# Kernel tuning notes

Hardware: AMD Instinct MI355X
Metric: run time of the kernel (lower is better)

Reference implementation:

```python
import jax, jax.numpy as jnp
import numpy as np

H = 16       # num_heads
DH = 64      # dim_head
SCALE = DH ** -0.5


def setup_inputs() -> dict:
    key = jax.random.key(0)
    k1, k2 = jax.random.split(key)
    ZT = jax.random.normal(k1, (2, 2048, 1024), dtype=jnp.float32)
    # Linear weight, shape (H*dh, dim); scaled like a typical init for stability
    W = jax.random.normal(k2, (1024, 1024), dtype=jnp.float32) * 0.02
    return {"ZT": ZT, "W": W}


def reference(ZT, W):
    b, n, dim = ZT.shape
    # UT(ZT): ZT @ W^T -> (b, n, H*dh), reshape to (b, h, n, dh)
    ZTU = jnp.einsum('bnd,ed->bne', ZT, W).reshape(b, n, H, DH).transpose(0, 2, 1, 3)
    # scores = ZTU @ ZTU^T * scale  (b, h, n, n)
    scores = jnp.einsum('bhnd,bhmd->bhnm', ZTU, ZTU) * SCALE
    attn = jax.nn.softmax(scores, axis=-1)  # dropout p=0 -> identity
    # attn @ ZTU -> (b, h, n, dh) -> (b, n, H*dh)
    ssa = jnp.einsum('bhnm,bhmd->bhnd', attn, ZTU)
    ssa = ssa.transpose(0, 2, 1, 3).reshape(b, n, H * DH)
    # UT(I).T == W (shape (H*dh, dim)); final projection back to dim
    mssa = jnp.einsum('bne,ed->bnd', ssa, W)
    # return_proj=False path: module returns (MSSA_out, MSSA_out)
    return (mssa, mssa)
```

## Files before the change

kernel.cpp:

```cpp
#include <hip/hip_runtime.h>
#include <hip/hip_bf16.h>
#include <stdint.h>

typedef __attribute__((ext_vector_type(8))) short bf16x8;
typedef __attribute__((ext_vector_type(4))) float f32x4;

#define MFMA16(a, b, c) __builtin_amdgcn_mfma_f32_16x16x32_bf16(a, b, c, 0, 0, 0)

typedef const __attribute__((address_space(1))) unsigned int* as1_u32p;
typedef __attribute__((address_space(3))) unsigned int* as3_u32p;
__device__ __forceinline__ void gl_lds16(const void* g, void* l) {
    __builtin_amdgcn_global_load_lds((as1_u32p)g, (as3_u32p)l, 16, 0, 0);
}

__device__ __forceinline__ unsigned short f2bs(float f) {
    __hip_bfloat16 h = __float2bfloat16(f);
    unsigned short s;
    __builtin_memcpy(&s, &h, 2);
    return s;
}

__device__ __forceinline__ unsigned int pk_bf16(float a, float b) {
    float2 f; f.x = a; f.y = b;
    __hip_bfloat162 h = __float22bfloat162_rn(f);
    unsigned int u;
    __builtin_memcpy(&u, &h, 4);
    return u;
}

__device__ __forceinline__ float exp2_raw(float x) {
    float r;
    asm("v_exp_f32 %0, %1" : "=v"(r) : "v"(x));
    return r;
}

#define QSCALE 0.18033688f

__global__ __launch_bounds__(256) void cvt_k(const float* __restrict__ w,
                                             const float* __restrict__ zt,
                                             unsigned short* __restrict__ wbf,
                                             unsigned short* __restrict__ wtbf,
                                             unsigned short* __restrict__ ztbf) {
    __shared__ __attribute__((aligned(16))) unsigned short T[64 * 72];
    const int tid = threadIdx.x;
    if (blockIdx.x >= 256) {
        const int i = ((int)blockIdx.x - 256) * 2048 + tid * 8;
        const float4 v0 = *(const float4*)(zt + i);
        const float4 v1 = *(const float4*)(zt + i + 4);
        uint4 wv;
        wv.x = pk_bf16(v0.x, v0.y);
        wv.y = pk_bf16(v0.z, v0.w);
        wv.z = pk_bf16(v1.x, v1.y);
        wv.w = pk_bf16(v1.z, v1.w);
        *(uint4*)(ztbf + i) = wv;
        return;
    }
    const int b2 = blockIdx.x;
    const int e0 = (b2 >> 4) * 64, d0 = (b2 & 15) * 64;
    const int el = tid >> 2;
    const int dl = (tid & 3) * 16;
    const float* src = w + (size_t)(e0 + el) * 1024 + d0 + dl;
    unsigned short myv[16];
#pragma unroll
    for (int q = 0; q < 4; ++q) {
        const float4 v = *(const float4*)(src + q * 4);
        myv[q * 4 + 0] = f2bs(v.x);
        myv[q * 4 + 1] = f2bs(v.y);
        myv[q * 4 + 2] = f2bs(v.z);
        myv[q * 4 + 3] = f2bs(v.w);
    }
    *(bf16x8*)(wbf + (size_t)(e0 + el) * 1024 + d0 + dl) = *(const bf16x8*)&myv[0];
    *(bf16x8*)(wbf + (size_t)(e0 + el) * 1024 + d0 + dl + 8) = *(const bf16x8*)&myv[8];
#pragma unroll
    for (int q = 0; q < 16; ++q) T[(dl + q) * 72 + el] = myv[q];
    __syncthreads();
#pragma unroll
    for (int p = 0; p < 2; ++p) {
        const int idx = p * 256 + tid;
        const int dd = idx >> 3, c = (idx & 7) * 8;
        const bf16x8 v = *(const bf16x8*)&T[dd * 72 + c];
        *(bf16x8*)(wtbf + (size_t)(d0 + dd) * 1024 + e0 + c) = v;
    }
}

template <int EPI>
__global__ __launch_bounds__(256, 2) void gemm_bt_k(
    const __hip_bfloat16* __restrict__ Abf, const __hip_bfloat16* __restrict__ B,
    unsigned short* __restrict__ ztu, unsigned short* __restrict__ ztut,
    float* __restrict__ out0, float* __restrict__ out1) {
    __shared__ __attribute__((aligned(16))) unsigned short smem[24576];
    unsigned short* Tb = smem;

    const int p = blockIdx.x;
    const int bm = (p & 7) * 8 + ((p >> 3) & 7);
    const int bn = p >> 6;
    const int tid = threadIdx.x;
    const int wave = tid >> 6, lane = tid & 63;
    const int wm = wave >> 1, wn = wave & 1;
    const int quad = lane >> 4, l16 = lane & 15;

    f32x4 acc[2][4] = {};

    const int lrow = lane >> 3;
    const int sw = (lane & 7) ^ lrow;
    const __hip_bfloat16* Ag0 = Abf + (size_t)(bm * 64 + (2 * wave) * 8 + lrow) * 1024 + sw * 8;
    const __hip_bfloat16* Ag1 = Ag0 + 8 * 1024;
    const __hip_bfloat16* Bg0 = B + (size_t)(bn * 128 + (4 * wave) * 8 + lrow) * 1024 + sw * 8;
    const __hip_bfloat16* Bg1 = Bg0 + 8 * 1024;
    const __hip_bfloat16* Bg2 = Bg0 + 16 * 1024;
    const __hip_bfloat16* Bg3 = Bg0 + 24 * 1024;

    auto stage = [&](int ko, unsigned short* sb) {
        gl_lds16(Ag0 + ko, sb + (2 * wave) * 512);
        gl_lds16(Ag1 + ko, sb + (2 * wave + 1) * 512);
        gl_lds16(Bg0 + ko, sb + 4096 + (4 * wave) * 512);
        gl_lds16(Bg1 + ko, sb + 4096 + (4 * wave + 1) * 512);
        gl_lds16(Bg2 + ko, sb + 4096 + (4 * wave + 2) * 512);
        gl_lds16(Bg3 + ko, sb + 4096 + (4 * wave + 3) * 512);
    };

    const int ch0 = (quad ^ (l16 & 7)) * 8;
    const int ch1 = ch0 ^ 32;
    const int raA = (wm * 32 + l16) * 64;
    const int raB = (wn * 64 + l16) * 64;

    stage(0, smem);
    __syncthreads();

    const int NIT = (EPI == 1) ? 32 : 16;
    for (int kt = 0; kt < NIT; ++kt) {
        unsigned short* const sb = smem + (kt & 1) * 12288;
        if (kt < NIT - 1) stage(((kt + 1) & 15) << 6, smem + (((kt & 1) ^ 1) * 12288));
        bf16x8 af[2][2], bfr[2][4];
#pragma unroll
        for (int i = 0; i < 2; ++i) {
            af[0][i] = *(const bf16x8*)&sb[raA + i * 1024 + ch0];
            af[1][i] = *(const bf16x8*)&sb[raA + i * 1024 + ch1];
        }
#pragma unroll
        for (int j = 0; j < 4; ++j) {
            bfr[0][j] = *(const bf16x8*)&sb[4096 + raB + j * 1024 + ch0];
            bfr[1][j] = *(const bf16x8*)&sb[4096 + raB + j * 1024 + ch1];
        }
#pragma unroll
        for (int h = 0; h < 2; ++h)
#pragma unroll
            for (int i = 0; i < 2; ++i)
#pragma unroll
                for (int j = 0; j < 4; ++j) acc[i][j] = MFMA16(af[h][i], bfr[h][j], acc[i][j]);
        __syncthreads();
    }

    if (EPI == 0) {
        const int h = bn * 2 + wn;
        const int bb = bm >> 5;
        const int nb = (bm & 31) * 64;
        const size_t hb = (size_t)(bb * 16 + h) * 131072;
#pragma unroll
        for (int i = 0; i < 2; ++i) {
#pragma unroll
            for (int r = 0; r < 4; ++r) {
                const int n = nb + wm * 32 + i * 16 + quad * 4 + r;
                uint2 pk;
                pk.x = pk_bf16(acc[i][0][r], acc[i][1][r]);
                pk.y = pk_bf16(acc[i][2][r], acc[i][3][r]);
                *(uint2*)(ztu + hb + n * 64 + l16 * 4) = pk;
                const int npl = wm * 32 + quad * 8 + i * 4 + r;
                Tb[(wn * 64 + 0 + l16) * 72 + npl] = (unsigned short)(pk.x & 0xffff);
                Tb[(wn * 64 + 16 + l16) * 72 + npl] = (unsigned short)(pk.x >> 16);
                Tb[(wn * 64 + 32 + l16) * 72 + npl] = (unsigned short)(pk.y & 0xffff);
                Tb[(wn * 64 + 48 + l16) * 72 + npl] = (unsigned short)(pk.y >> 16);
            }
        }
        __syncthreads();
#pragma unroll
        for (int ee = 0; ee < 4; ++ee) {
            const int e_local = wave * 32 + ee * 8 + (lane >> 3);
            const int nc = (lane & 7) * 8;
            const bf16x8 v = *(const bf16x8*)&Tb[e_local * 72 + nc];
            const int hh = bn * 2 + (e_local >> 6);
            const int dh = e_local & 63;
            *(bf16x8*)(ztut + (size_t)(bb * 16 + hh) * 131072 + dh * 2048 + nb + nc) = v;
        }
    } else {
#pragma unroll
        for (int i = 0; i < 2; ++i) {
#pragma unroll
            for (int r = 0; r < 4; ++r) {
                const int mm = bm * 64 + wm * 32 + i * 16 + quad * 4 + r;
#pragma unroll
                for (int j = 0; j < 4; ++j) {
                    const int e = bn * 128 + wn * 64 + j * 16 + l16;
                    const float v = acc[i][j][r] * 0.5f;
                    out0[(size_t)mm * 1024 + e] = v;
                    out1[(size_t)mm * 1024 + e] = v;
                }
            }
        }
    }
}

__global__ __launch_bounds__(256, 2) void attn_k(const unsigned short* __restrict__ ztu,
                                                 const unsigned short* __restrict__ ztut,
                                                 unsigned short* __restrict__ ssa) {
    __shared__ __attribute__((aligned(16))) unsigned short Kt[64 * 64];
    __shared__ __attribute__((aligned(16))) unsigned short Vt[64 * 64];
    const int p = blockIdx.x;
    const int ii = p >> 3;
    const int bh = (p & 7) * 4 + (ii >> 4);
    const int qt = ii & 15;
    const int tid = threadIdx.x, wave = tid >> 6, lane = tid & 63;
    const int quad = lane >> 4, l16 = lane & 15;
    const unsigned short* base = ztu + (size_t)bh * 131072;
    const unsigned short* baseT = ztut + (size_t)bh * 131072;

    const int qb = qt * 128 + wave * 32;
    bf16x8 qa[2][2];
#pragma unroll
    for (int g = 0; g < 2; ++g) {
        qa[g][0] = *(const bf16x8*)(base + (qb + g * 16 + l16) * 64 + quad * 8);
        qa[g][1] = *(const bf16x8*)(base + (qb + g * 16 + l16) * 64 + 32 + quad * 8);
    }

    f32x4 o[2][4] = {};
    f32x4 lacc[2] = {};
    bf16x8 ones;
#pragma unroll
    for (int z = 0; z < 8; ++z) ones[z] = (short)0x3f80;

    const int c0 = wave * 2, c1 = c0 + 1;
    const int lrow = lane >> 3;
    const int sw = (lane & 7) ^ lrow;
    const unsigned short* gK0 = base + (c0 * 8 + lrow) * 64 + sw * 8;
    const unsigned short* gK1 = base + (c1 * 8 + lrow) * 64 + sw * 8;
    const unsigned short* gV0 = baseT + (size_t)(c0 * 8 + lrow) * 2048 + sw * 8;
    const unsigned short* gV1 = baseT + (size_t)(c1 * 8 + lrow) * 2048 + sw * 8;
    unsigned short* lK0 = &Kt[c0 * 512];
    unsigned short* lK1 = &Kt[c1 * 512];
    unsigned short* lV0 = &Vt[c0 * 512];
    unsigned short* lV1 = &Vt[c1 * 512];

    const int swq = (quad ^ (l16 & 7));
    const int koff0 = l16 * 64 + swq * 8;
    const int koff1 = l16 * 64 + (swq ^ 4) * 8;

    for (int t = 0; t < 32; ++t) {
        gl_lds16(gK0 + t * 4096, lK0);
        gl_lds16(gK1 + t * 4096, lK1);
        gl_lds16(gV0 + t * 64, lV0);
        gl_lds16(gV1 + t * 64, lV1);
        __syncthreads();

        f32x4 st[2][4];
#pragma unroll
        for (int nf = 0; nf < 4; ++nf) {
            bf16x8 kb0 = *(const bf16x8*)&Kt[nf * 1024 + koff0];
            bf16x8 kb1 = *(const bf16x8*)&Kt[nf * 1024 + koff1];
#pragma unroll
            for (int g = 0; g < 2; ++g) {
                f32x4 z = {0.f, 0.f, 0.f, 0.f};
                z = MFMA16(kb0, qa[g][0], z);
                z = MFMA16(kb1, qa[g][1], z);
                st[g][nf] = z;
            }
        }

        bf16x8 pa[2][2];
#pragma unroll
        for (int g = 0; g < 2; ++g) {
            float e[16];
#pragma unroll
            for (int nf = 0; nf < 4; ++nf)
#pragma unroll
                for (int r = 0; r < 4; ++r) e[nf * 4 + r] = exp2_raw(st[g][nf][r] * QSCALE);
            uint4 u0, u1;
            u0.x = pk_bf16(e[0], e[1]);   u0.y = pk_bf16(e[2], e[3]);
            u0.z = pk_bf16(e[4], e[5]);   u0.w = pk_bf16(e[6], e[7]);
            u1.x = pk_bf16(e[8], e[9]);   u1.y = pk_bf16(e[10], e[11]);
            u1.z = pk_bf16(e[12], e[13]); u1.w = pk_bf16(e[14], e[15]);
            __builtin_memcpy(&pa[g][0], &u0, 16);
            __builtin_memcpy(&pa[g][1], &u1, 16);
            lacc[g] = MFMA16(ones, pa[g][0], lacc[g]);
            lacc[g] = MFMA16(ones, pa[g][1], lacc[g]);
        }

#pragma unroll
        for (int df = 0; df < 4; ++df) {
            bf16x8 vb0 = *(const bf16x8*)&Vt[df * 1024 + koff0];
            bf16x8 vb1 = *(const bf16x8*)&Vt[df * 1024 + koff1];
#pragma unroll
            for (int g = 0; g < 2; ++g) {
                o[g][df] = MFMA16(vb0, pa[g][0], o[g][df]);
                o[g][df] = MFMA16(vb1, pa[g][1], o[g][df]);
            }
        }
        __syncthreads();
    }

    const int b = bh >> 4, h = bh & 15;
#pragma unroll
    for (int g = 0; g < 2; ++g) {
        const float inv = 1.0f / lacc[g][0];
        const int token = b * 2048 + qb + g * 16 + l16;
#pragma unroll
        for (int df = 0; df < 4; ++df) {
            uint2 pk;
            pk.x = pk_bf16(o[g][df][0] * inv, o[g][df][1] * inv);
            pk.y = pk_bf16(o[g][df][2] * inv, o[g][df][3] * inv);
            *(uint2*)(ssa + (size_t)token * 1024 + h * 64 + df * 16 + quad * 4) = pk;
        }
    }
}

extern "C" void kernel_launch(void* const* d_in, const int* in_sizes, int n_in,
                              void* d_out, int out_size, void* d_ws, size_t ws_size,
                              hipStream_t stream) {
    const float* ZT = (const float*)d_in[0];
    const float* W = (const float*)d_in[1];
    float* out = (float*)d_out;
    char* ws = (char*)d_ws;

    unsigned short* wbf   = (unsigned short*)(ws);
    unsigned short* wtbf  = (unsigned short*)(ws + 2u * 1024 * 1024);
    unsigned short* ztu   = (unsigned short*)(ws + 4u * 1024 * 1024);
    unsigned short* ztut  = (unsigned short*)(ws + 12u * 1024 * 1024);
    unsigned short* scr20 = (unsigned short*)(ws + 20u * 1024 * 1024);

    cvt_k<<<2304, 256, 0, stream>>>(W, ZT, wbf, wtbf, scr20);
    gemm_bt_k<0><<<512, 256, 0, stream>>>((const __hip_bfloat16*)scr20,
                                          (const __hip_bfloat16*)wbf, ztu, ztut,
                                          nullptr, nullptr);
    attn_k<<<512, 256, 0, stream>>>(ztu, ztut, scr20);
    gemm_bt_k<1><<<512, 256, 0, stream>>>((const __hip_bfloat16*)scr20,
                                          (const __hip_bfloat16*)wtbf, nullptr, nullptr,
                                          out, out + 4194304);
}
```

Measured before the change: 155.3 us.

## Drop redundant K pass in output GEMM, stage stores via LDS, shrink attention blocks

The output-projection GEMM previously looped over K twice (wrapping the K index) and scaled by 0.5. It now runs a single 16-step K loop, halving that GEMM's MFMA and load work. Its epilogue now writes accumulators into a padded LDS tile and stores both outputs with coalesced float4 writes instead of scattered scalar stores. The attention kernel moves to 128-thread blocks covering 64 queries each, with twice as many blocks. That improves occupancy and load balance, but each K/V tile loaded into LDS is now reused by half as many queries.

Measured after the change: 155.7 us. Within noise of the previous version (+0.2%).

```diff
diff --git a/kernel.cpp b/kernel.cpp
--- a/kernel.cpp
+++ b/kernel.cpp
@@ -127,10 +127,9 @@
     stage(0, smem);
     __syncthreads();
 
-    const int NIT = (EPI == 1) ? 32 : 16;
-    for (int kt = 0; kt < NIT; ++kt) {
+    for (int kt = 0; kt < 16; ++kt) {
         unsigned short* const sb = smem + (kt & 1) * 12288;
-        if (kt < NIT - 1) stage(((kt + 1) & 15) << 6, smem + (((kt & 1) ^ 1) * 12288));
+        if (kt < 15) stage((kt + 1) << 6, smem + (((kt & 1) ^ 1) * 12288));
         bf16x8 af[2][2], bfr[2][4];
 #pragma unroll
         for (int i = 0; i < 2; ++i) {
@@ -183,38 +182,45 @@
             *(bf16x8*)(ztut + (size_t)(bb * 16 + hh) * 131072 + dh * 2048 + nb + nc) = v;
         }
     } else {
-#pragma unroll
-        for (int i = 0; i < 2; ++i) {
+        float* Tf = (float*)smem;
+#pragma unroll
+        for (int i = 0; i < 2; ++i)
 #pragma unroll
             for (int r = 0; r < 4; ++r) {
-                const int mm = bm * 64 + wm * 32 + i * 16 + quad * 4 + r;
-#pragma unroll
-                for (int j = 0; j < 4; ++j) {
-                    const int e = bn * 128 + wn * 64 + j * 16 + l16;
-                    const float v = acc[i][j][r] * 0.5f;
-                    out0[(size_t)mm * 1024 + e] = v;
-                    out1[(size_t)mm * 1024 + e] = v;
-                }
+                const int ml = wm * 32 + i * 16 + quad * 4 + r;
+#pragma unroll
+                for (int j = 0; j < 4; ++j)
+                    Tf[ml * 132 + wn * 64 + j * 16 + l16] = acc[i][j][r];
             }
-        }
-    }
-}
-
-__global__ __launch_bounds__(256, 2) void attn_k(const unsigned short* __restrict__ ztu,
+        __syncthreads();
+#pragma unroll
+        for (int q = 0; q < 8; ++q) {
+            const int idx = q * 256 + tid;
+            const int row = idx >> 5;
+            const int c4 = (idx & 31) * 4;
+            const float4 v = *(const float4*)&Tf[row * 132 + c4];
+            const size_t off = (size_t)(bm * 64 + row) * 1024 + bn * 128 + c4;
+            *(float4*)(out0 + off) = v;
+            *(float4*)(out1 + off) = v;
+        }
+    }
+}
+
+__global__ __launch_bounds__(128, 2) void attn_k(const unsigned short* __restrict__ ztu,
                                                  const unsigned short* __restrict__ ztut,
                                                  unsigned short* __restrict__ ssa) {
     __shared__ __attribute__((aligned(16))) unsigned short Kt[64 * 64];
     __shared__ __attribute__((aligned(16))) unsigned short Vt[64 * 64];
     const int p = blockIdx.x;
     const int ii = p >> 3;
-    const int bh = (p & 7) * 4 + (ii >> 4);
-    const int qt = ii & 15;
+    const int bh = (p & 7) * 4 + (ii >> 5);
+    const int qt = ii & 31;
     const int tid = threadIdx.x, wave = tid >> 6, lane = tid & 63;
     const int quad = lane >> 4, l16 = lane & 15;
     const unsigned short* base = ztu + (size_t)bh * 131072;
     const unsigned short* baseT = ztut + (size_t)bh * 131072;
 
-    const int qb = qt * 128 + wave * 32;
+    const int qb = qt * 64 + wave * 32;
     bf16x8 qa[2][2];
 #pragma unroll
     for (int g = 0; g < 2; ++g) {
@@ -228,34 +234,38 @@
 #pragma unroll
     for (int z = 0; z < 8; ++z) ones[z] = (short)0x3f80;
 
-    const int c0 = wave * 2, c1 = c0 + 1;
     const int lrow = lane >> 3;
     const int sw = (lane & 7) ^ lrow;
-    const unsigned short* gK0 = base + (c0 * 8 + lrow) * 64 + sw * 8;
-    const unsigned short* gK1 = base + (c1 * 8 + lrow) * 64 + sw * 8;
-    const unsigned short* gV0 = baseT + (size_t)(c0 * 8 + lrow) * 2048 + sw * 8;
-    const unsigned short* gV1 = baseT + (size_t)(c1 * 8 + lrow) * 2048 + sw * 8;
-    unsigned short* lK0 = &Kt[c0 * 512];
-    unsigned short* lK1 = &Kt[c1 * 512];
-    unsigned short* lV0 = &Vt[c0 * 512];
-    unsigned short* lV1 = &Vt[c1 * 512];
+    const unsigned short* gK[4];
+    const unsigned short* gV[4];
+    unsigned short* lK[4];
+    unsigned short* lV[4];
+#pragma unroll
+    for (int j = 0; j < 4; ++j) {
+        const int c = wave * 4 + j;
+        gK[j] = base + (c * 8 + lrow) * 64 + sw * 8;
+        gV[j] = baseT + (size_t)(c * 8 + lrow) * 2048 + sw * 8;
+        lK[j] = &Kt[c * 512];
+        lV[j] = &Vt[c * 512];
+    }
 
     const int swq = (quad ^ (l16 & 7));
     const int koff0 = l16 * 64 + swq * 8;
     const int koff1 = l16 * 64 + (swq ^ 4) * 8;
 
     for (int t = 0; t < 32; ++t) {
-        gl_lds16(gK0 + t * 4096, lK0);
-        gl_lds16(gK1 + t * 4096, lK1);
-        gl_lds16(gV0 + t * 64, lV0);
-        gl_lds16(gV1 + t * 64, lV1);
+#pragma unroll
+        for (int j = 0; j < 4; ++j) {
+            gl_lds16(gK[j] + t * 4096, lK[j]);
+            gl_lds16(gV[j] + t * 64, lV[j]);
+        }
         __syncthreads();
 
         f32x4 st[2][4];
 #pragma unroll
         for (int nf = 0; nf < 4; ++nf) {
-            bf16x8 kb0 = *(const bf16x8*)&Kt[nf * 1024 + koff0];
-            bf16x8 kb1 = *(const bf16x8*)&Kt[nf * 1024 + koff1];
+            const bf16x8 kb0 = *(const bf16x8*)&Kt[nf * 1024 + koff0];
+            const bf16x8 kb1 = *(const bf16x8*)&Kt[nf * 1024 + koff1];
 #pragma unroll
             for (int g = 0; g < 2; ++g) {
                 f32x4 z = {0.f, 0.f, 0.f, 0.f};
@@ -286,8 +296,8 @@
 
 #pragma unroll
         for (int df = 0; df < 4; ++df) {
-            bf16x8 vb0 = *(const bf16x8*)&Vt[df * 1024 + koff0];
-            bf16x8 vb1 = *(const bf16x8*)&Vt[df * 1024 + koff1];
+            const bf16x8 vb0 = *(const bf16x8*)&Vt[df * 1024 + koff0];
+            const bf16x8 vb1 = *(const bf16x8*)&Vt[df * 1024 + koff1];
 #pragma unroll
             for (int g = 0; g < 2; ++g) {
                 o[g][df] = MFMA16(vb0, pa[g][0], o[g][df]);
@@ -330,7 +340,7 @@
     gemm_bt_k<0><<<512, 256, 0, stream>>>((const __hip_bfloat16*)scr20,
                                           (const __hip_bfloat16*)wbf, ztu, ztut,
                                           nullptr, nullptr);
-    attn_k<<<512, 256, 0, stream>>>(ztu, ztut, scr20);
+    attn_k<<<1024, 128, 0, stream>>>(ztu, ztut, scr20);
     gemm_bt_k<1><<<512, 256, 0, stream>>>((const __hip_bfloat16*)scr20,
                                           (const __hip_bfloat16*)wtbf, nullptr, nullptr,
                                           out, out + 4194304);
```
